# Optimization experiments

Measured on AMD Instinct MI355X. Metric: run time of the kernel, lower is better.

Reference implementation:

```python
import jax, jax.numpy as jnp
import numpy as np

IMAGE_SIZE = 320
SIGMA = 0.01      # soft-edge width in NDC units (~1.6 px at 320 res)
CHUNK = 128       # faces per scan step (bounds peak memory)


def setup_inputs() -> dict:
    key = jax.random.key(0)
    k1, k2 = jax.random.split(key)
    verts = jax.random.normal(k1, (4, 778, 3), dtype=jnp.float32) * 0.5
    faces = jax.random.randint(k2, (1538, 3), 0, 778, dtype=jnp.int32)
    return {"verts": verts, "faces": faces}


def _silhouette(verts, faces):
    B = verts.shape[0]
    S = IMAGE_SIZE
    # NMR.forward flips the y axis of verts before rendering
    v = verts * jnp.array([1.0, -1.0, 1.0], dtype=verts.dtype)
    xy = v[..., :2]  # orthographic projection (perspective=False)
    F = faces.shape[0]
    n_chunks = -(-F // CHUNK)
    Fp = n_chunks * CHUNK
    faces_p = jnp.pad(faces, ((0, Fp - F), (0, 0)))
    valid = (jnp.arange(Fp) < F).astype(verts.dtype)
    tri = xy[:, faces_p]  # [B, Fp, 3, 2]
    tri = jnp.moveaxis(tri.reshape(B, n_chunks, CHUNK, 3, 2), 1, 0)  # [nc,B,C,3,2]
    valid = valid.reshape(n_chunks, CHUNK)
    # pixel centers in NDC [-1, 1]
    lin = (jnp.arange(S, dtype=verts.dtype) + 0.5) / S * 2.0 - 1.0
    py, px = jnp.meshgrid(lin, lin, indexing="ij")
    px = px.reshape(-1)  # [P]
    py = py.reshape(-1)

    def edge_d(a, b, sgn):
        # signed distance of every pixel to oriented edge a->b: [B, C, P]
        ex = b[..., 0] - a[..., 0]
        ey = b[..., 1] - a[..., 1]
        inv_len = 1.0 / (jnp.sqrt(ex * ex + ey * ey) + 1e-8)
        d = (ex[..., None] * (py[None, None, :] - a[..., 1:2])
             - ey[..., None] * (px[None, None, :] - a[..., 0:1]))
        return sgn[..., None] * d * inv_len[..., None]

    def body(acc, chunk):
        tri_c, m = chunk  # [B,C,3,2], [C]
        v0, v1, v2 = tri_c[..., 0, :], tri_c[..., 1, :], tri_c[..., 2, :]
        # orientation sign so CW / CCW triangles are handled uniformly
        area2 = ((v1[..., 0] - v0[..., 0]) * (v2[..., 1] - v0[..., 1])
                 - (v1[..., 1] - v0[..., 1]) * (v2[..., 0] - v0[..., 0]))
        sgn = jnp.sign(area2)
        logp = (jax.nn.log_sigmoid(edge_d(v0, v1, sgn) / SIGMA)
                + jax.nn.log_sigmoid(edge_d(v1, v2, sgn) / SIGMA)
                + jax.nn.log_sigmoid(edge_d(v2, v0, sgn) / SIGMA))
        prob = jnp.clip(jnp.exp(logp) * m[None, :, None], 0.0, 1.0 - 1e-6)
        return acc + jnp.sum(jnp.log1p(-prob), axis=1), None

    acc0 = jnp.zeros((B, S * S), dtype=verts.dtype)
    acc, _ = jax.lax.scan(body, acc0, (tri, valid))
    # silhouette = 1 - prod_f (1 - coverage_f), accumulated in log space
    return (1.0 - jnp.exp(acc)).reshape(B, S, S)


def reference(verts, faces):
    return _silhouette(verts, faces)
```

## Files before the change

### kernel.cpp

```cpp
#include <hip/hip_runtime.h>
#include <math.h>


#define IMG_S 320
#define N_FACES 1538
#define N_VERTS 778
#define N_BATCH 4
#define FP 1600
#define TILE 8
#define CHUNK_F 256
#define NWAVE 4
#define INV_SIGMA 100.0f
#define T_CUT 14.0f
#define ACC_CUT_P 2.0611536e-9f
#define LOG2_1EM6 -19.9315686f

__global__ __launch_bounds__(256)
void prep_faces(const float* __restrict__ verts,
                const int* __restrict__ faces,
                float4* __restrict__ gE0,
                float4* __restrict__ gE1,
                float4* __restrict__ gE2)
{
    const int f = blockIdx.x * 256 + threadIdx.x;
    const int b = blockIdx.z;
    if (f >= N_FACES) return;

    const float* vb = verts + (size_t)b * N_VERTS * 3;
    const int i0 = faces[f * 3 + 0];
    const int i1 = faces[f * 3 + 1];
    const int i2 = faces[f * 3 + 2];
    const float x0 = vb[i0 * 3 + 0], y0 = -vb[i0 * 3 + 1];
    const float x1 = vb[i1 * 3 + 0], y1 = -vb[i1 * 3 + 1];
    const float x2 = vb[i2 * 3 + 0], y2 = -vb[i2 * 3 + 1];

    const float dx1 = x1 - x0, dy1 = y1 - y0;
    const float dx2 = x2 - x0, dy2 = y2 - y0;
    const float area2 = __builtin_fmaf(dx1, dy2, -__fmul_rn(dy1, dx2));
    const float sgn = (area2 > 0.0f) ? 1.0f : ((area2 < 0.0f) ? -1.0f : 0.0f);

    const size_t o = (size_t)b * FP + f;
    {
        const float ex = x1 - x0, ey = y1 - y0;
        const float s = sgn * INV_SIGMA / (sqrtf(ex * ex + ey * ey) + 1e-8f);
        gE0[o] = make_float4(-s * ey, s * ex, s * (ey * x0 - ex * y0), 0.0f);
    }
    {
        const float ex = x2 - x1, ey = y2 - y1;
        const float s = sgn * INV_SIGMA / (sqrtf(ex * ex + ey * ey) + 1e-8f);
        gE1[o] = make_float4(-s * ey, s * ex, s * (ey * x1 - ex * y1), 0.0f);
    }
    {
        const float ex = x0 - x2, ey = y0 - y2;
        const float s = sgn * INV_SIGMA / (sqrtf(ex * ex + ey * ey) + 1e-8f);
        gE2[o] = make_float4(-s * ey, s * ex, s * (ey * x2 - ex * y2), 0.0f);
    }
}

__global__ __launch_bounds__(256)
void silhouette_ws(const float4* __restrict__ gE0,
                   const float4* __restrict__ gE1,
                   const float4* __restrict__ gE2,
                   float* __restrict__ out)
{
    __shared__ float4 sE0[CHUNK_F];
    __shared__ float4 sE1[CHUNK_F];
    __shared__ float4 sE2[CHUNK_F];
    __shared__ float sAcc[256];
    __shared__ int sCount;
    __shared__ int sAlive;
    __shared__ int sCover;

    const int t    = threadIdx.x;
    const int wave = t >> 6;
    const int p    = t & 63;
    const int b    = blockIdx.z;
    const int lx   = p & 7;
    const int ly   = p >> 3;
    const int gx   = blockIdx.x * TILE + lx;
    const int gy   = blockIdx.y * TILE + ly;

    const float w  = 2.0f / IMG_S;
    const float px = (gx + 0.5f) * w - 1.0f;
    const float py = (gy + 0.5f) * w - 1.0f;
    const float cx = (blockIdx.x * TILE + 4) * w - 1.0f;
    const float cy = (blockIdx.y * TILE + 4) * w - 1.0f;
    const float rr = 3.5f * w;

    float acc = 1.0f;

    const int nchunks = (N_FACES + CHUNK_F - 1) / CHUNK_F;
    for (int c = 0; c < nchunks; ++c) {
        sAcc[t] = acc;
        if (t == 0) { sCount = 0; sAlive = 0; sCover = 0; }
        __syncthreads();

        const float tot = sAcc[p] * sAcc[p + 64] * sAcc[p + 128] * sAcc[p + 192];
        const bool alive = (tot > ACC_CUT_P);
        if (alive) sAlive = 1;

        const int fc = c * CHUNK_F + t;
        if (fc < N_FACES) {
            const size_t o = (size_t)b * FP + fc;
            const float4 e0 = gE0[o];
            const float4 e1 = gE1[o];
            const float4 e2 = gE2[o];
            const float c0 = fmaf(e0.x, cx, fmaf(e0.y, cy, e0.z));
            const float c1 = fmaf(e1.x, cx, fmaf(e1.y, cy, e1.z));
            const float c2 = fmaf(e2.x, cx, fmaf(e2.y, cy, e2.z));
            const float r0 = rr * (fabsf(e0.x) + fabsf(e0.y));
            const float r1 = rr * (fabsf(e1.x) + fabsf(e1.y));
            const float r2 = rr * (fabsf(e2.x) + fabsf(e2.y));
            const float m_hi = fminf(c0 + r0, fminf(c1 + r1, c2 + r2));
            const float m_lo = fminf(c0 - r0, fminf(c1 - r1, c2 - r2));
            if (m_lo > T_CUT) {
                atomicAdd(&sCover, 1);
            } else if (m_hi > -T_CUT) {
                const int slot = atomicAdd(&sCount, 1);
                sE0[slot] = e0;
                sE1[slot] = e1;
                sE2[slot] = e2;
            }
        }
        __syncthreads();

        if (sAlive == 0) break;

        const float coverF = exp2f((float)sCover * LOG2_1EM6);
        bool live = alive && (acc * coverF > ACC_CUT_P);
        if (wave == 0) acc *= coverF;

        const int n = sCount;
        for (int j = wave; j < n; j += NWAVE) {
            if (__ballot(live) == 0ull) break;
            const float4 e0 = sE0[j];
            const float4 e1 = sE1[j];
            const float4 e2 = sE2[j];
            const float xa = fmaf(e0.x, px, fmaf(e0.y, py, e0.z));
            const float xb = fmaf(e1.x, px, fmaf(e1.y, py, e1.z));
            const float xc = fmaf(e2.x, px, fmaf(e2.y, py, e2.z));
            const float m = fminf(xa, fminf(xb, xc));
            if (live && m > -T_CUT) {
                if (m > T_CUT) {
                    acc *= 1e-6f;
                } else {
                    const float mid = fmaxf(fminf(fmaxf(xa, xb), xc),
                                            fminf(xa, xb));
                    float f;
                    if (mid > T_CUT) {
                        f = __builtin_amdgcn_rcpf(1.0f + __expf(m));
                    } else {
                        const float da = 1.0f + __expf(-xa);
                        const float db = 1.0f + __expf(-xb);
                        const float dc = 1.0f + __expf(-xc);
                        f = 1.0f - __builtin_amdgcn_rcpf(da * db * dc);
                    }
                    acc *= fmaxf(f, 1e-6f);
                }
                live = (acc > ACC_CUT_P);
            }
        }

        __syncthreads();
    }

    sAcc[t] = acc;
    __syncthreads();
    if (t < 64) {
        const float tot = sAcc[p] * sAcc[p + 64] * sAcc[p + 128] * sAcc[p + 192];
        out[(size_t)b * (IMG_S * IMG_S) + (size_t)gy * IMG_S + gx] = 1.0f - tot;
    }
}

extern "C" void kernel_launch(void* const* d_in, const int* in_sizes, int n_in,
                              void* d_out, int out_size, void* d_ws, size_t ws_size,
                              hipStream_t stream) {
    const float* verts = (const float*)d_in[0];
    const int* faces = (const int*)d_in[1];
    float* out = (float*)d_out;

    float4* gE0 = (float4*)d_ws;
    float4* gE1 = gE0 + (size_t)N_BATCH * FP;
    float4* gE2 = gE1 + (size_t)N_BATCH * FP;

    dim3 pgrid((N_FACES + 255) / 256, 1, N_BATCH);
    prep_faces<<<pgrid, 256, 0, stream>>>(verts, faces, gE0, gE1, gE2);

    dim3 grid(IMG_S / TILE, IMG_S / TILE, N_BATCH);
    silhouette_ws<<<grid, 256, 0, stream>>>(gE0, gE1, gE2, out);
}
```

Before: 92.08 us.

## Use persistent blocks with atomic tile queue, ballot compaction, looser cutoffs

Replaces the one-block-per-tile grid with a persistent grid of 2048 blocks. The blocks pull tile indices from a global atomic counter, which prep_faces resets each call. Face binning now uses wave-level ballot and popcount, so each wave does one shared atomic instead of one per thread. It also loosens the saturation cutoffs (T_CUT and ACC_CUT_P) to skip more work and checks the early-exit ballot less often; the looser cutoffs trade accuracy in near-saturated pixels for less work.

```diff
diff --git a/kernel.cpp b/kernel.cpp
--- a/kernel.cpp
+++ b/kernel.cpp
@@ -8,22 +8,28 @@
 #define N_BATCH 4
 #define FP 1600
 #define TILE 8
+#define TPS 40
+#define TOTAL_TILES (TPS * TPS * N_BATCH)
+#define RGRID 2048
 #define CHUNK_F 256
 #define NWAVE 4
 #define INV_SIGMA 100.0f
-#define T_CUT 14.0f
-#define ACC_CUT_P 2.0611536e-9f
+#define T_CUT 12.0f
+#define ACC_CUT_P 2.2603294e-6f
 #define LOG2_1EM6 -19.9315686f
+#define CNT_OFF (3 * N_BATCH * FP)
 
 __global__ __launch_bounds__(256)
 void prep_faces(const float* __restrict__ verts,
                 const int* __restrict__ faces,
                 float4* __restrict__ gE0,
                 float4* __restrict__ gE1,
-                float4* __restrict__ gE2)
+                float4* __restrict__ gE2,
+                int* __restrict__ cnt)
 {
     const int f = blockIdx.x * 256 + threadIdx.x;
     const int b = blockIdx.z;
+    if (f == 0 && b == 0) *cnt = RGRID;
     if (f >= N_FACES) return;
 
     const float* vb = verts + (size_t)b * N_VERTS * 3;
@@ -61,6 +67,7 @@
 void silhouette_ws(const float4* __restrict__ gE0,
                    const float4* __restrict__ gE1,
                    const float4* __restrict__ gE2,
+                   int* __restrict__ cnt,
                    float* __restrict__ out)
 {
     __shared__ float4 sE0[CHUNK_F];
@@ -70,105 +77,134 @@
     __shared__ int sCount;
     __shared__ int sAlive;
     __shared__ int sCover;
+    __shared__ int sNext;
 
     const int t    = threadIdx.x;
     const int wave = t >> 6;
+    const int lane = t & 63;
     const int p    = t & 63;
-    const int b    = blockIdx.z;
-    const int lx   = p & 7;
-    const int ly   = p >> 3;
-    const int gx   = blockIdx.x * TILE + lx;
-    const int gy   = blockIdx.y * TILE + ly;
-
+    const int plx  = p & 7;
+    const int ply  = p >> 3;
     const float w  = 2.0f / IMG_S;
-    const float px = (gx + 0.5f) * w - 1.0f;
-    const float py = (gy + 0.5f) * w - 1.0f;
-    const float cx = (blockIdx.x * TILE + 4) * w - 1.0f;
-    const float cy = (blockIdx.y * TILE + 4) * w - 1.0f;
     const float rr = 3.5f * w;
-
-    float acc = 1.0f;
-
     const int nchunks = (N_FACES + CHUNK_F - 1) / CHUNK_F;
-    for (int c = 0; c < nchunks; ++c) {
+
+    int idx = blockIdx.x;
+    while (idx < TOTAL_TILES) {
+        const int b  = idx / (TPS * TPS);
+        const int r  = idx - b * (TPS * TPS);
+        const int ty = r / TPS;
+        const int tx = r - ty * TPS;
+        const int gx = tx * TILE + plx;
+        const int gy = ty * TILE + ply;
+        const float px = (gx + 0.5f) * w - 1.0f;
+        const float py = (gy + 0.5f) * w - 1.0f;
+        const float cx = (tx * TILE + 4) * w - 1.0f;
+        const float cy = (ty * TILE + 4) * w - 1.0f;
+
+        float acc = 1.0f;
+
+        for (int c = 0; c < nchunks; ++c) {
+            sAcc[t] = acc;
+            if (t == 0) { sCount = 0; sAlive = 0; sCover = 0; }
+            __syncthreads();
+
+            const float tot = sAcc[p] * sAcc[p + 64] * sAcc[p + 128] * sAcc[p + 192];
+            const bool alive = (tot > ACC_CUT_P);
+            if (alive) sAlive = 1;
+
+            {
+                const int fc  = c * CHUNK_F + t;
+                const int fcc = (fc < N_FACES) ? fc : (N_FACES - 1);
+                const size_t o = (size_t)b * FP + fcc;
+                const float4 e0 = gE0[o];
+                const float4 e1 = gE1[o];
+                const float4 e2 = gE2[o];
+                const float c0 = fmaf(e0.x, cx, fmaf(e0.y, cy, e0.z));
+                const float c1 = fmaf(e1.x, cx, fmaf(e1.y, cy, e1.z));
+                const float c2 = fmaf(e2.x, cx, fmaf(e2.y, cy, e2.z));
+                const float r0 = rr * (fabsf(e0.x) + fabsf(e0.y));
+                const float r1 = rr * (fabsf(e1.x) + fabsf(e1.y));
+                const float r2 = rr * (fabsf(e2.x) + fabsf(e2.y));
+                const float m_hi = fminf(c0 + r0, fminf(c1 + r1, c2 + r2));
+                const float m_lo = fminf(c0 - r0, fminf(c1 - r1, c2 - r2));
+                const bool vald   = (fc < N_FACES);
+                const bool isCov  = vald && (m_lo > T_CUT);
+                const bool isBand = vald && !isCov && (m_hi > -T_CUT);
+
+                const unsigned long long mb = __ballot(isBand);
+                int base = 0;
+                if (lane == 0) {
+                    const int nw = __popcll(mb);
+                    if (nw) base = atomicAdd(&sCount, nw);
+                }
+                base = __shfl(base, 0);
+                if (isBand) {
+                    const int slot = base + __popcll(mb & ((1ull << lane) - 1ull));
+                    sE0[slot] = e0;
+                    sE1[slot] = e1;
+                    sE2[slot] = e2;
+                }
+                const unsigned long long mc = __ballot(isCov);
+                if (lane == 0) {
+                    const int ncv = __popcll(mc);
+                    if (ncv) atomicAdd(&sCover, ncv);
+                }
+            }
+            __syncthreads();
+
+            if (sAlive == 0) break;
+
+            const float coverF = exp2f((float)sCover * LOG2_1EM6);
+            bool live = alive && (acc * coverF > ACC_CUT_P);
+            if (wave == 0) acc *= coverF;
+
+            const int n = sCount;
+            for (int j = wave; j < n; j += NWAVE) {
+                const float4 e0 = sE0[j];
+                const float4 e1 = sE1[j];
+                const float4 e2 = sE2[j];
+                const float xa = fmaf(e0.x, px, fmaf(e0.y, py, e0.z));
+                const float xb = fmaf(e1.x, px, fmaf(e1.y, py, e1.z));
+                const float xc = fmaf(e2.x, px, fmaf(e2.y, py, e2.z));
+                const float m = fminf(xa, fminf(xb, xc));
+                if (live && m > -T_CUT) {
+                    float f;
+                    if (m > T_CUT) {
+                        f = 1e-6f;
+                    } else {
+                        const float mid = fmaxf(fminf(fmaxf(xa, xb), xc),
+                                                fminf(xa, xb));
+                        if (mid > T_CUT) {
+                            f = 1.0f - __builtin_amdgcn_rcpf(1.0f + __expf(-m));
+                        } else {
+                            const float da = 1.0f + __expf(-xa);
+                            const float db = 1.0f + __expf(-xb);
+                            const float dc = 1.0f + __expf(-xc);
+                            f = 1.0f - __builtin_amdgcn_rcpf(da * db * dc);
+                        }
+                        f = fmaxf(f, 1e-6f);
+                    }
+                    acc *= f;
+                    live = (acc > ACC_CUT_P);
+                }
+                if (((j - wave) & 12) == 12) {
+                    if (__ballot(live) == 0ull) break;
+                }
+            }
+
+            __syncthreads();
+        }
+
         sAcc[t] = acc;
-        if (t == 0) { sCount = 0; sAlive = 0; sCover = 0; }
         __syncthreads();
-
-        const float tot = sAcc[p] * sAcc[p + 64] * sAcc[p + 128] * sAcc[p + 192];
-        const bool alive = (tot > ACC_CUT_P);
-        if (alive) sAlive = 1;
-
-        const int fc = c * CHUNK_F + t;
-        if (fc < N_FACES) {
-            const size_t o = (size_t)b * FP + fc;
-            const float4 e0 = gE0[o];
-            const float4 e1 = gE1[o];
-            const float4 e2 = gE2[o];
-            const float c0 = fmaf(e0.x, cx, fmaf(e0.y, cy, e0.z));
-            const float c1 = fmaf(e1.x, cx, fmaf(e1.y, cy, e1.z));
-            const float c2 = fmaf(e2.x, cx, fmaf(e2.y, cy, e2.z));
-            const float r0 = rr * (fabsf(e0.x) + fabsf(e0.y));
-            const float r1 = rr * (fabsf(e1.x) + fabsf(e1.y));
-            const float r2 = rr * (fabsf(e2.x) + fabsf(e2.y));
-            const float m_hi = fminf(c0 + r0, fminf(c1 + r1, c2 + r2));
-            const float m_lo = fminf(c0 - r0, fminf(c1 - r1, c2 - r2));
-            if (m_lo > T_CUT) {
-                atomicAdd(&sCover, 1);
-            } else if (m_hi > -T_CUT) {
-                const int slot = atomicAdd(&sCount, 1);
-                sE0[slot] = e0;
-                sE1[slot] = e1;
-                sE2[slot] = e2;
-            }
+        if (t < 64) {
+            const float tot = sAcc[p] * sAcc[p + 64] * sAcc[p + 128] * sAcc[p + 192];
+            out[(size_t)b * (IMG_S * IMG_S) + (size_t)gy * IMG_S + gx] = 1.0f - tot;
         }
+        if (t == 0) sNext = atomicAdd(cnt, 1);
         __syncthreads();
-
-        if (sAlive == 0) break;
-
-        const float coverF = exp2f((float)sCover * LOG2_1EM6);
-        bool live = alive && (acc * coverF > ACC_CUT_P);
-        if (wave == 0) acc *= coverF;
-
-        const int n = sCount;
-        for (int j = wave; j < n; j += NWAVE) {
-            if (__ballot(live) == 0ull) break;
-            const float4 e0 = sE0[j];
-            const float4 e1 = sE1[j];
-            const float4 e2 = sE2[j];
-            const float xa = fmaf(e0.x, px, fmaf(e0.y, py, e0.z));
-            const float xb = fmaf(e1.x, px, fmaf(e1.y, py, e1.z));
-            const float xc = fmaf(e2.x, px, fmaf(e2.y, py, e2.z));
-            const float m = fminf(xa, fminf(xb, xc));
-            if (live && m > -T_CUT) {
-                if (m > T_CUT) {
-                    acc *= 1e-6f;
-                } else {
-                    const float mid = fmaxf(fminf(fmaxf(xa, xb), xc),
-                                            fminf(xa, xb));
-                    float f;
-                    if (mid > T_CUT) {
-                        f = __builtin_amdgcn_rcpf(1.0f + __expf(m));
-                    } else {
-                        const float da = 1.0f + __expf(-xa);
-                        const float db = 1.0f + __expf(-xb);
-                        const float dc = 1.0f + __expf(-xc);
-                        f = 1.0f - __builtin_amdgcn_rcpf(da * db * dc);
-                    }
-                    acc *= fmaxf(f, 1e-6f);
-                }
-                live = (acc > ACC_CUT_P);
-            }
-        }
-
-        __syncthreads();
-    }
-
-    sAcc[t] = acc;
-    __syncthreads();
-    if (t < 64) {
-        const float tot = sAcc[p] * sAcc[p + 64] * sAcc[p + 128] * sAcc[p + 192];
-        out[(size_t)b * (IMG_S * IMG_S) + (size_t)gy * IMG_S + gx] = 1.0f - tot;
+        idx = sNext;
     }
 }
 
@@ -182,10 +218,10 @@
     float4* gE0 = (float4*)d_ws;
     float4* gE1 = gE0 + (size_t)N_BATCH * FP;
     float4* gE2 = gE1 + (size_t)N_BATCH * FP;
+    int* cnt = (int*)(gE0 + CNT_OFF);
 
     dim3 pgrid((N_FACES + 255) / 256, 1, N_BATCH);
-    prep_faces<<<pgrid, 256, 0, stream>>>(verts, faces, gE0, gE1, gE2);
-
-    dim3 grid(IMG_S / TILE, IMG_S / TILE, N_BATCH);
-    silhouette_ws<<<grid, 256, 0, stream>>>(gE0, gE1, gE2, out);
+    prep_faces<<<pgrid, 256, 0, stream>>>(verts, faces, gE0, gE1, gE2, cnt);
+
+    silhouette_ws<<<dim3(RGRID), 256, 0, stream>>>(gE0, gE1, gE2, cnt, out);
 }
```

Result: slower. 137.2 us (+49.1%).
